# Performance work log

Measured on AMD Instinct MI355X. Metric: run time of the kernel, lower is better.

Reference implementation:

```python
import jax, jax.numpy as jnp
import numpy as np

B, NQ, NK, D = 8, 2048, 2048, 1024

def setup_inputs() -> dict:
    key = jax.random.key(0)
    k1, k2, k3, k4, k5 = jax.random.split(key, 5)
    query_input = jax.random.normal(k1, (B, NQ, D), dtype=jnp.float32)
    key_input = jax.random.normal(k2, (B, NK, D), dtype=jnp.float32)
    s = 1.0 / np.sqrt(D)
    # nn.Linear(in,out,bias=False): y = x @ W.T, W shape (out,in)
    Wq = jax.random.uniform(k3, (D, D), dtype=jnp.float32, minval=-s, maxval=s)
    Wk = jax.random.uniform(k4, (D, D), dtype=jnp.float32, minval=-s, maxval=s)
    Wv = jax.random.uniform(k5, (D, D), dtype=jnp.float32, minval=-s, maxval=s)
    return {"query_input": query_input, "key_input": key_input,
            "Wq": Wq, "Wk": Wk, "Wv": Wv}

def reference(query_input, key_input, Wq, Wk, Wv):
    d = query_input.shape[-1]
    q = jnp.einsum('bnd,ed->bne', query_input, Wq)   # (b, n_q, d)
    k = jnp.einsum('bmd,ed->bme', key_input, Wk)     # (b, n_k, d)
    v = jnp.einsum('bnd,ed->bne', query_input, Wv)   # (b, n_q, d) -- value from query_input
    # scores: K @ Q^T -> (b, n_k, n_q), softmax over n_q
    a = jnp.einsum('bmd,bnd->bmn', k, q) / jnp.sqrt(jnp.float32(d))
    a = jax.nn.softmax(a, axis=-1)
    context = jnp.einsum('bmn,bnd->bmd', a, v)       # (b, n_k, d)
    return context + key_input
```

## Files before the change

kernel.cpp:

```cpp
#include <hip/hip_runtime.h>
#include <hip/hip_bf16.h>

using bf16 = __bf16;
typedef __bf16 bf16x8 __attribute__((ext_vector_type(8)));
typedef float f32x4 __attribute__((ext_vector_type(4)));

__device__ __forceinline__ void gload_lds16(const bf16* g, bf16* l) {
  __builtin_amdgcn_global_load_lds(
      (const __attribute__((address_space(1))) void*)g,
      (__attribute__((address_space(3))) void*)l, 16, 0, 0);
}

__global__ __launch_bounds__(256) void cvt_f32_bf16(const float* __restrict__ in,
                                                    bf16* __restrict__ out, int n) {
  int i = (blockIdx.x * 256 + threadIdx.x) * 8;
  if (i >= n) return;
  float4 f0 = *(const float4*)&in[i];
  float4 f1 = *(const float4*)&in[i + 4];
  bf16x8 o;
  o[0] = (bf16)f0.x; o[1] = (bf16)f0.y; o[2] = (bf16)f0.z; o[3] = (bf16)f0.w;
  o[4] = (bf16)f1.x; o[5] = (bf16)f1.y; o[6] = (bf16)f1.z; o[7] = (bf16)f1.w;
  *(bf16x8*)&out[i] = o;
}

__global__ __launch_bounds__(256) void tcvt_f32_bf16(const float* __restrict__ in,
                                                     bf16* __restrict__ out,
                                                     int R, int C) {
  __shared__ float tile[64][65];
  const int t = threadIdx.x;
  const int r0 = blockIdx.y * 64, c0 = blockIdx.x * 64;
  const int r = t >> 4, c4 = (t & 15) * 4;
#pragma unroll
  for (int rr = 0; rr < 64; rr += 16) {
    float4 v = *(const float4*)&in[(long)(r0 + r + rr) * C + c0 + c4];
    tile[r + rr][c4 + 0] = v.x; tile[r + rr][c4 + 1] = v.y;
    tile[r + rr][c4 + 2] = v.z; tile[r + rr][c4 + 3] = v.w;
  }
  __syncthreads();
  const int cc = t >> 2, rseg = (t & 3) * 16;
  bf16 tmp[16];
#pragma unroll
  for (int k = 0; k < 16; ++k) tmp[k] = (bf16)tile[rseg + k][cc];
  *(bf16x8*)&out[(long)(c0 + cc) * R + r0 + rseg] = *(bf16x8*)&tmp[0];
  *(bf16x8*)&out[(long)(c0 + cc) * R + r0 + rseg + 8] = *(bf16x8*)&tmp[8];
}

__global__ __launch_bounds__(256) void zero_f32(float* __restrict__ p, int n) {
  int i = (blockIdx.x * 256 + threadIdx.x) * 4;
  if (i < n) *(float4*)&p[i] = make_float4(0.f, 0.f, 0.f, 0.f);
}

__global__ __launch_bounds__(256)
void gemm_small_atomic(const bf16* __restrict__ A, const bf16* __restrict__ B,
                       float* __restrict__ C, int lda, int ldb, int ldc) {
  const int tid = threadIdx.x;
  const int wave = tid >> 6;
  const int lane = tid & 63;
  const int wr = wave >> 1, wc = wave & 1;
  const long brow = (long)blockIdx.x * 128;
  const long bcol = (long)blockIdx.y * 128;
  const int kofs = blockIdx.z * 256;

  __shared__ bf16 As[128 * 32];
  __shared__ bf16 Bs[128 * 32];
  f32x4 acc[4][4] = {};

  const int r0 = tid >> 2;
  const int c0 = (tid & 3) * 8;
  const bf16* ga = A + (brow + r0) * (long)lda + kofs + c0;
  const bf16* gb = B + (bcol + r0) * (long)ldb + kofs + c0;
  bf16* la0 = As + tid * 8;
  bf16* la1 = As + 2048 + tid * 8;
  bf16* lb0 = Bs + tid * 8;
  bf16* lb1 = Bs + 2048 + tid * 8;
  const int afo = (wr * 64 + (lane & 15)) * 32 + (lane >> 4) * 8;
  const int bfo = (wc * 64 + (lane & 15)) * 32 + (lane >> 4) * 8;

  for (int kt = 0; kt < 8; ++kt) {
    gload_lds16(ga, la0);
    gload_lds16(ga + (long)64 * lda, la1);
    gload_lds16(gb, lb0);
    gload_lds16(gb + (long)64 * ldb, lb1);
    ga += 32; gb += 32;
    __syncthreads();
    bf16x8 av[4], bv[4];
#pragma unroll
    for (int i = 0; i < 4; ++i) {
      av[i] = *(const bf16x8*)&As[afo + i * 512];
      bv[i] = *(const bf16x8*)&Bs[bfo + i * 512];
    }
#pragma unroll
    for (int mi = 0; mi < 4; ++mi)
#pragma unroll
      for (int ni = 0; ni < 4; ++ni)
        acc[mi][ni] = __builtin_amdgcn_mfma_f32_16x16x32_bf16(av[mi], bv[ni],
                                                              acc[mi][ni], 0, 0, 0);
    __syncthreads();
  }

  const int or0 = wr * 64 + ((lane >> 4) << 2);
  const int oc0 = wc * 64 + (lane & 15);
#pragma unroll
  for (int mi = 0; mi < 4; ++mi)
#pragma unroll
    for (int ni = 0; ni < 4; ++ni)
#pragma unroll
      for (int j = 0; j < 4; ++j) {
        const long row = brow + or0 + mi * 16 + j;
        const long col = bcol + oc0 + ni * 16;
        atomicAdd(&C[row * ldc + col], acc[mi][ni][j]);
      }
}

__device__ __forceinline__ void load_frags(const bf16* __restrict__ buf,
                                           int wr, int wc, int lk, int lr,
                                           bf16x8 (&R)[12]) {
#pragma unroll
  for (int mi = 0; mi < 8; ++mi) {
    const int r = wr * 128 + mi * 16 + lr;
    R[mi] = *(const bf16x8*)&buf[r * 32 + ((lk ^ ((r >> 1) & 3)) << 3)];
  }
#pragma unroll
  for (int ni = 0; ni < 4; ++ni) {
    const int r = wc * 64 + ni * 16 + lr;
    R[8 + ni] = *(const bf16x8*)&buf[8192 + r * 32 + ((lk ^ ((r >> 1) & 3)) << 3)];
  }
}

__device__ __forceinline__ void mfma_tile(const bf16x8 (&R)[12], f32x4 (&acc)[8][4]) {
  __builtin_amdgcn_s_setprio(1);
#pragma unroll
  for (int mi = 0; mi < 8; ++mi)
#pragma unroll
    for (int ni = 0; ni < 4; ++ni)
      acc[mi][ni] = __builtin_amdgcn_mfma_f32_16x16x32_bf16(R[mi], R[8 + ni], acc[mi][ni], 0, 0, 0);
  __builtin_amdgcn_s_setprio(0);
}

template <int EPI>
__global__ __launch_bounds__(512, 2)
void gemm_bt(const bf16* __restrict__ A, const bf16* __restrict__ B,
             void* __restrict__ Cv, const bf16* __restrict__ Add,
             const float* __restrict__ Inv,
             int K, int lda, int ldb, int ldc,
             long sA, long sB, long sC, long sAdd, float scale) {
  int bx = blockIdx.x, by = blockIdx.y, bz = blockIdx.z;
  if (gridDim.z > 1) {
    const int gx = gridDim.x, gxy = gx * gridDim.y;
    const int nwg = gxy * gridDim.z;
    int lin = bx + gx * by + gxy * bz;
    lin = (lin & 7) * (nwg >> 3) + (lin >> 3);
    bz = lin / gxy; const int rem = lin - bz * gxy;
    by = rem / gx;  bx = rem - by * gx;
  }
  A += (long)bz * sA;
  B += (long)bz * sB;
  const int tid = threadIdx.x;
  const int lane = tid & 63;
  const int wave = tid >> 6;
  const int wr = wave >> 2;
  const int wc = wave & 3;
  const long brow = (long)bx * 256;
  const long bcol = (long)by * 256;

  __shared__ bf16 lds[4][16384];

  f32x4 acc[8][4] = {};

  const int srow = tid >> 2;
  const int scg  = (tid & 3) ^ ((srow >> 1) & 3);
  const bf16* gA = A + (brow + srow) * (long)lda + scg * 8;
  const bf16* gB = B + (bcol + srow) * (long)ldb + scg * 8;
  const long a128 = (long)lda << 7;
  const long b128 = (long)ldb << 7;

  const int nk = K >> 5;

  auto stage = [&](int t) {
    bf16* buf = (bf16*)lds[t & 3];
    const bf16* a = gA + (long)t * 32;
    const bf16* b = gB + (long)t * 32;
    gload_lds16(a,        buf + tid * 8);
    gload_lds16(a + a128, buf + 4096 + tid * 8);
    gload_lds16(b,        buf + 8192 + tid * 8);
    gload_lds16(b + b128, buf + 12288 + tid * 8);
  };

  const int lk = lane >> 4;
  const int lr = lane & 15;

  stage(0); stage(1); stage(2);
  asm volatile("s_waitcnt vmcnt(4)" ::: "memory");
  __builtin_amdgcn_s_barrier();

  bf16x8 R0[12], R1[12];
  load_frags((const bf16*)lds[0], wr, wc, lk, lr, R0);

  for (int t = 0; t < nk; t += 2) {
    load_frags((const bf16*)lds[(t + 1) & 3], wr, wc, lk, lr, R1);
    if (t + 3 < nk) stage(t + 3);
    mfma_tile(R0, acc);
    if (t + 3 < nk) { asm volatile("s_waitcnt vmcnt(4)" ::: "memory"); }
    else            { asm volatile("s_waitcnt vmcnt(0)" ::: "memory"); }
    __builtin_amdgcn_s_barrier();
    if (t + 2 < nk) load_frags((const bf16*)lds[(t + 2) & 3], wr, wc, lk, lr, R0);
    if (t + 4 < nk) stage(t + 4);
    mfma_tile(R1, acc);
    if (t + 4 < nk) { asm volatile("s_waitcnt vmcnt(4)" ::: "memory"); }
    else            { asm volatile("s_waitcnt vmcnt(0)" ::: "memory"); }
    __builtin_amdgcn_s_barrier();
  }

  const int or0 = wr * 128 + ((lane >> 4) << 2);
  const int oc0 = wc * 64 + (lane & 15);
#pragma unroll
  for (int mi = 0; mi < 8; ++mi) {
#pragma unroll
    for (int ni = 0; ni < 4; ++ni) {
#pragma unroll
      for (int j = 0; j < 4; ++j) {
        const long row = brow + or0 + mi * 16 + j;
        const long col = bcol + oc0 + ni * 16;
        if constexpr (EPI == 0) {
          bf16* C = (bf16*)Cv + (long)bz * sC;
          C[row * ldc + col] = (bf16)(acc[mi][ni][j] * scale);
        } else if constexpr (EPI == 1) {
          bf16* C = (bf16*)Cv + (long)bz * sC;
          C[row * ldc + col] = (bf16)__expf(acc[mi][ni][j] * scale);
        } else {
          float* C = (float*)Cv + (long)bz * sC;
          const bf16* Ad = Add + (long)bz * sAdd;
          const float* iv = Inv + (long)bz * 2048;
          C[row * ldc + col] = acc[mi][ni][j] * iv[row] + (float)Ad[row * ldc + col];
        }
      }
    }
  }
}

__global__ __launch_bounds__(256) void rowsum_inv(const bf16* __restrict__ E,
                                                  float* __restrict__ inv) {
  const long row = blockIdx.x;
  const bf16* p = E + row * 2048;
  const int tid = threadIdx.x;
  bf16x8 v = *(const bf16x8*)&p[tid * 8];
  float s = 0.f;
#pragma unroll
  for (int i = 0; i < 8; ++i) s += (float)v[i];
#pragma unroll
  for (int off = 32; off > 0; off >>= 1) s += __shfl_xor(s, off, 64);
  __shared__ float red[4];
  if ((tid & 63) == 0) red[tid >> 6] = s;
  __syncthreads();
  if (tid == 0) inv[row] = 1.0f / (red[0] + red[1] + red[2] + red[3]);
}

extern "C" void kernel_launch(void* const* d_in, const int* in_sizes, int n_in,
                              void* d_out, int out_size, void* d_ws, size_t ws_size,
                              hipStream_t stream) {
  const float* q_in = (const float*)d_in[0];
  const float* k_in = (const float*)d_in[1];
  const float* Wq   = (const float*)d_in[2];
  const float* Wk   = (const float*)d_in[3];
  const float* Wv   = (const float*)d_in[4];
  float* out = (float*)d_out;
  char* ws = (char*)d_ws;

  bf16*  qb   = (bf16*)(ws);
  bf16*  kb   = (bf16*)(ws + 33554432);
  bf16*  S    = (bf16*)(ws + 67108864);
  float* GTf  = (float*)(ws + 67108864);
  bf16*  GTb  = (bf16*)(ws + 71303168);
  bf16*  T1   = (bf16*)(ws + 134217728);
  bf16*  Vpt  = (bf16*)(ws + 134217728);
  bf16*  Wvb  = (bf16*)(ws + 167772160);
  bf16*  WqTb = (bf16*)(ws + 169869312);
  bf16*  WkTb = (bf16*)(ws + 171966464);
  float* inv  = (float*)(ws + 169869312);

  zero_f32<<<1024, 256, 0, stream>>>(GTf, 1048576);
  tcvt_f32_bf16<<<dim3(16, 16), 256, 0, stream>>>(Wq, WqTb, 1024, 1024);
  tcvt_f32_bf16<<<dim3(16, 16), 256, 0, stream>>>(Wk, WkTb, 1024, 1024);
  cvt_f32_bf16<<<8192, 256, 0, stream>>>(q_in, qb, 16777216);
  cvt_f32_bf16<<<8192, 256, 0, stream>>>(k_in, kb, 16777216);
  cvt_f32_bf16<<<512, 256, 0, stream>>>(Wv, Wvb, 1048576);

  gemm_small_atomic<<<dim3(8, 8, 4), 256, 0, stream>>>(WqTb, WkTb, GTf, 1024, 1024, 1024);
  cvt_f32_bf16<<<512, 256, 0, stream>>>(GTf, GTb, 1048576);

  gemm_bt<0><<<dim3(64, 4, 1), 512, 0, stream>>>(
      kb, GTb, T1, nullptr, nullptr, 1024, 1024, 1024, 1024, 0, 0, 0, 0, 1.0f);

  gemm_bt<1><<<dim3(8, 8, 8), 512, 0, stream>>>(
      T1, qb, S, nullptr, nullptr, 1024, 1024, 1024, 2048,
      2097152L, 2097152L, 4194304L, 0L, 0.03125f);

  gemm_bt<0><<<dim3(4, 8, 8), 512, 0, stream>>>(
      Wvb, qb, Vpt, nullptr, nullptr, 1024, 1024, 1024, 2048,
      0L, 2097152L, 2097152L, 0L, 1.0f);

  rowsum_inv<<<16384, 256, 0, stream>>>(S, inv);

  gemm_bt<2><<<dim3(8, 4, 8), 512, 0, stream>>>(
      S, Vpt, out, kb, inv, 2048, 2048, 2048, 1024,
      4194304L, 2097152L, 2097152L, 2097152L, 1.0f);
}
```

Measured before the change: 298.6 us.

## Shrink GEMM tiles to 128x128 and fuse softmax row sums into exp epilogue

Measured after the change: 335.2 us. 1.12x slower.

```diff
diff --git a/kernel.cpp b/kernel.cpp
--- a/kernel.cpp
+++ b/kernel.cpp
@@ -114,34 +114,34 @@
 
 __device__ __forceinline__ void load_frags(const bf16* __restrict__ buf,
                                            int wr, int wc, int lk, int lr,
-                                           bf16x8 (&R)[12]) {
-#pragma unroll
-  for (int mi = 0; mi < 8; ++mi) {
-    const int r = wr * 128 + mi * 16 + lr;
+                                           bf16x8 (&R)[8]) {
+#pragma unroll
+  for (int mi = 0; mi < 4; ++mi) {
+    const int r = wr * 64 + mi * 16 + lr;
     R[mi] = *(const bf16x8*)&buf[r * 32 + ((lk ^ ((r >> 1) & 3)) << 3)];
   }
 #pragma unroll
   for (int ni = 0; ni < 4; ++ni) {
     const int r = wc * 64 + ni * 16 + lr;
-    R[8 + ni] = *(const bf16x8*)&buf[8192 + r * 32 + ((lk ^ ((r >> 1) & 3)) << 3)];
-  }
-}
-
-__device__ __forceinline__ void mfma_tile(const bf16x8 (&R)[12], f32x4 (&acc)[8][4]) {
+    R[4 + ni] = *(const bf16x8*)&buf[4096 + r * 32 + ((lk ^ ((r >> 1) & 3)) << 3)];
+  }
+}
+
+__device__ __forceinline__ void mfma_tile(const bf16x8 (&R)[8], f32x4 (&acc)[4][4]) {
   __builtin_amdgcn_s_setprio(1);
 #pragma unroll
-  for (int mi = 0; mi < 8; ++mi)
+  for (int mi = 0; mi < 4; ++mi)
 #pragma unroll
     for (int ni = 0; ni < 4; ++ni)
-      acc[mi][ni] = __builtin_amdgcn_mfma_f32_16x16x32_bf16(R[mi], R[8 + ni], acc[mi][ni], 0, 0, 0);
+      acc[mi][ni] = __builtin_amdgcn_mfma_f32_16x16x32_bf16(R[mi], R[4 + ni], acc[mi][ni], 0, 0, 0);
   __builtin_amdgcn_s_setprio(0);
 }
 
 template <int EPI>
-__global__ __launch_bounds__(512, 2)
+__global__ __launch_bounds__(256, 2)
 void gemm_bt(const bf16* __restrict__ A, const bf16* __restrict__ B,
              void* __restrict__ Cv, const bf16* __restrict__ Add,
-             const float* __restrict__ Inv,
+             float* __restrict__ RS,
              int K, int lda, int ldb, int ldc,
              long sA, long sB, long sC, long sAdd, float scale) {
   int bx = blockIdx.x, by = blockIdx.y, bz = blockIdx.z;
@@ -158,21 +158,21 @@
   const int tid = threadIdx.x;
   const int lane = tid & 63;
   const int wave = tid >> 6;
-  const int wr = wave >> 2;
-  const int wc = wave & 3;
-  const long brow = (long)bx * 256;
-  const long bcol = (long)by * 256;
-
-  __shared__ bf16 lds[4][16384];
-
-  f32x4 acc[8][4] = {};
+  const int wr = wave >> 1;
+  const int wc = wave & 1;
+  const long brow = (long)bx * 128;
+  const long bcol = (long)by * 128;
+
+  __shared__ bf16 lds[4][8192];
+
+  f32x4 acc[4][4] = {};
 
   const int srow = tid >> 2;
   const int scg  = (tid & 3) ^ ((srow >> 1) & 3);
   const bf16* gA = A + (brow + srow) * (long)lda + scg * 8;
   const bf16* gB = B + (bcol + srow) * (long)ldb + scg * 8;
-  const long a128 = (long)lda << 7;
-  const long b128 = (long)ldb << 7;
+  const long a64 = (long)lda << 6;
+  const long b64 = (long)ldb << 6;
 
   const int nk = K >> 5;
 
@@ -180,10 +180,10 @@
     bf16* buf = (bf16*)lds[t & 3];
     const bf16* a = gA + (long)t * 32;
     const bf16* b = gB + (long)t * 32;
-    gload_lds16(a,        buf + tid * 8);
-    gload_lds16(a + a128, buf + 4096 + tid * 8);
-    gload_lds16(b,        buf + 8192 + tid * 8);
-    gload_lds16(b + b128, buf + 12288 + tid * 8);
+    gload_lds16(a,       buf + tid * 8);
+    gload_lds16(a + a64, buf + 2048 + tid * 8);
+    gload_lds16(b,       buf + 4096 + tid * 8);
+    gload_lds16(b + b64, buf + 6144 + tid * 8);
   };
 
   const int lk = lane >> 4;
@@ -193,7 +193,7 @@
   asm volatile("s_waitcnt vmcnt(4)" ::: "memory");
   __builtin_amdgcn_s_barrier();
 
-  bf16x8 R0[12], R1[12];
+  bf16x8 R0[8], R1[8];
   load_frags((const bf16*)lds[0], wr, wc, lk, lr, R0);
 
   for (int t = 0; t < nk; t += 2) {
@@ -211,48 +211,42 @@
     __builtin_amdgcn_s_barrier();
   }
 
-  const int or0 = wr * 128 + ((lane >> 4) << 2);
+  const int or0 = wr * 64 + ((lane >> 4) << 2);
   const int oc0 = wc * 64 + (lane & 15);
 #pragma unroll
-  for (int mi = 0; mi < 8; ++mi) {
-#pragma unroll
-    for (int ni = 0; ni < 4; ++ni) {
-#pragma unroll
-      for (int j = 0; j < 4; ++j) {
-        const long row = brow + or0 + mi * 16 + j;
-        const long col = bcol + oc0 + ni * 16;
-        if constexpr (EPI == 0) {
-          bf16* C = (bf16*)Cv + (long)bz * sC;
-          C[row * ldc + col] = (bf16)(acc[mi][ni][j] * scale);
-        } else if constexpr (EPI == 1) {
-          bf16* C = (bf16*)Cv + (long)bz * sC;
-          C[row * ldc + col] = (bf16)__expf(acc[mi][ni][j] * scale);
-        } else {
-          float* C = (float*)Cv + (long)bz * sC;
-          const bf16* Ad = Add + (long)bz * sAdd;
-          const float* iv = Inv + (long)bz * 2048;
-          C[row * ldc + col] = acc[mi][ni][j] * iv[row] + (float)Ad[row * ldc + col];
+  for (int mi = 0; mi < 4; ++mi) {
+#pragma unroll
+    for (int j = 0; j < 4; ++j) {
+      const long row = brow + or0 + mi * 16 + j;
+      if constexpr (EPI == 0) {
+        bf16* C = (bf16*)Cv + (long)bz * sC;
+#pragma unroll
+        for (int ni = 0; ni < 4; ++ni)
+          C[row * ldc + bcol + oc0 + ni * 16] = (bf16)(acc[mi][ni][j] * scale);
+      } else if constexpr (EPI == 1) {
+        bf16* C = (bf16*)Cv + (long)bz * sC;
+        float s = 0.f;
+#pragma unroll
+        for (int ni = 0; ni < 4; ++ni) {
+          const float e = __expf(acc[mi][ni][j] * scale);
+          s += e;
+          C[row * ldc + bcol + oc0 + ni * 16] = (bf16)e;
+        }
+        s += __shfl_xor(s, 1, 64); s += __shfl_xor(s, 2, 64);
+        s += __shfl_xor(s, 4, 64); s += __shfl_xor(s, 8, 64);
+        if ((lane & 15) == 0) atomicAdd(&RS[(long)bz * 2048 + row], s);
+      } else {
+        float* C = (float*)Cv + (long)bz * sC;
+        const bf16* Ad = Add + (long)bz * sAdd;
+        const float iv = 1.0f / RS[(long)bz * 2048 + row];
+#pragma unroll
+        for (int ni = 0; ni < 4; ++ni) {
+          const long col = bcol + oc0 + ni * 16;
+          C[row * ldc + col] = acc[mi][ni][j] * iv + (float)Ad[row * ldc + col];
         }
       }
     }
   }
-}
-
-__global__ __launch_bounds__(256) void rowsum_inv(const bf16* __restrict__ E,
-                                                  float* __restrict__ inv) {
-  const long row = blockIdx.x;
-  const bf16* p = E + row * 2048;
-  const int tid = threadIdx.x;
-  bf16x8 v = *(const bf16x8*)&p[tid * 8];
-  float s = 0.f;
-#pragma unroll
-  for (int i = 0; i < 8; ++i) s += (float)v[i];
-#pragma unroll
-  for (int off = 32; off > 0; off >>= 1) s += __shfl_xor(s, off, 64);
-  __shared__ float red[4];
-  if ((tid & 63) == 0) red[tid >> 6] = s;
-  __syncthreads();
-  if (tid == 0) inv[row] = 1.0f / (red[0] + red[1] + red[2] + red[3]);
 }
 
 extern "C" void kernel_launch(void* const* d_in, const int* in_sizes, int n_in,
@@ -276,7 +270,7 @@
   bf16*  Wvb  = (bf16*)(ws + 167772160);
   bf16*  WqTb = (bf16*)(ws + 169869312);
   bf16*  WkTb = (bf16*)(ws + 171966464);
-  float* inv  = (float*)(ws + 169869312);
+  float* rs   = (float*)(ws + 169869312);
 
   zero_f32<<<1024, 256, 0, stream>>>(GTf, 1048576);
   tcvt_f32_bf16<<<dim3(16, 16), 256, 0, stream>>>(Wq, WqTb, 1024, 1024);
@@ -287,21 +281,20 @@
 
   gemm_small_atomic<<<dim3(8, 8, 4), 256, 0, stream>>>(WqTb, WkTb, GTf, 1024, 1024, 1024);
   cvt_f32_bf16<<<512, 256, 0, stream>>>(GTf, GTb, 1048576);
-
-  gemm_bt<0><<<dim3(64, 4, 1), 512, 0, stream>>>(
+  zero_f32<<<16, 256, 0, stream>>>(rs, 16384);
+
+  gemm_bt<0><<<dim3(128, 8, 1), 256, 0, stream>>>(
       kb, GTb, T1, nullptr, nullptr, 1024, 1024, 1024, 1024, 0, 0, 0, 0, 1.0f);
 
-  gemm_bt<1><<<dim3(8, 8, 8), 512, 0, stream>>>(
-      T1, qb, S, nullptr, nullptr, 1024, 1024, 1024, 2048,
+  gemm_bt<1><<<dim3(16, 16, 8), 256, 0, stream>>>(
+      T1, qb, S, nullptr, rs, 1024, 1024, 1024, 2048,
       2097152L, 2097152L, 4194304L, 0L, 0.03125f);
 
-  gemm_bt<0><<<dim3(4, 8, 8), 512, 0, stream>>>(
+  gemm_bt<0><<<dim3(8, 16, 8), 256, 0, stream>>>(
       Wvb, qb, Vpt, nullptr, nullptr, 1024, 1024, 1024, 2048,
       0L, 2097152L, 2097152L, 0L, 1.0f);
 
-  rowsum_inv<<<16384, 256, 0, stream>>>(S, inv);
-
-  gemm_bt<2><<<dim3(8, 4, 8), 512, 0, stream>>>(
-      S, Vpt, out, kb, inv, 2048, 2048, 2048, 1024,
+  gemm_bt<2><<<dim3(16, 8, 8), 256, 0, stream>>>(
+      S, Vpt, out, kb, rs, 2048, 2048, 2048, 1024,
       4194304L, 2097152L, 2097152L, 2097152L, 1.0f);
 }
```
